# Kernel tuning notes

Hardware: AMD Instinct MI355X
Metric: run time of the kernel (lower is better)

The kernel has to match this reference:

```python
import jax, jax.numpy as jnp
import numpy as np

P = 8192          # number of gaussians
H = 256           # image height
W = 256           # image width
TANX = 0.5        # tan(fovx/2)
TANY = 0.5        # tan(fovy/2)
SCALE_MOD = 1.0
CHUNK = 128       # gaussians composited per scan step
FX = W / (2.0 * TANX)   # focal_x, as in forward()
FY = H / (2.0 * TANY)   # focal_y


def setup_inputs() -> dict:
    key = jax.random.key(0)
    k = jax.random.split(key, 6)
    # place gaussians in the camera frustum (camera at origin, looking +z)
    z = jax.random.uniform(k[0], (P,), minval=2.0, maxval=6.0)
    xy = jax.random.normal(k[1], (P, 2)) * 0.4 * (z * TANX)[:, None]
    means3D = jnp.concatenate([xy, z[:, None]], axis=1)
    scales = 0.01 + 0.04 * jax.random.uniform(k[2], (P, 3))
    rotations = jax.random.normal(k[3], (P, 4))  # normalized inside reference
    opacities = 0.05 + 0.9 * jax.random.uniform(k[4], (P, 1))
    colors_precomp = jax.random.uniform(k[5], (P, 3))
    background = jnp.zeros((3,), jnp.float32)
    viewmatrix = jnp.eye(4, dtype=jnp.float32)  # row-vector convention: p' = [p,1] @ V
    znear, zfar = 0.01, 100.0
    Pm = np.zeros((4, 4), np.float32)
    Pm[0, 0] = 1.0 / TANX
    Pm[1, 1] = 1.0 / TANY
    Pm[2, 2] = zfar / (zfar - znear)
    Pm[2, 3] = -(zfar * znear) / (zfar - znear)
    Pm[3, 2] = 1.0
    projmatrix = jnp.asarray(Pm.T)  # row-vector convention (full proj = proj @ view, view = I)
    return dict(means3D=means3D, colors_precomp=colors_precomp, opacities=opacities,
                scales=scales, rotations=rotations, background=background,
                viewmatrix=viewmatrix, projmatrix=projmatrix)


def _quat_to_rot(q):
    q = q / jnp.linalg.norm(q, axis=-1, keepdims=True)
    r, x, y, z = q[:, 0], q[:, 1], q[:, 2], q[:, 3]
    R = jnp.stack([
        1 - 2 * (y * y + z * z), 2 * (x * y - r * z), 2 * (x * z + r * y),
        2 * (x * y + r * z), 1 - 2 * (x * x + z * z), 2 * (y * z - r * x),
        2 * (x * z - r * y), 2 * (y * z + r * x), 1 - 2 * (x * x + y * y)], axis=-1)
    return R.reshape(-1, 3, 3)


def _forward(means3D, colors_precomp, opacities, scales, rotations, background,
             viewmatrix, projmatrix):
    Pn = means3D.shape[0]
    # --- preprocess: 3D covariance from scale/rotation ---
    R = _quat_to_rot(rotations)
    s2 = (scales * SCALE_MOD) ** 2
    Sigma = jnp.einsum('pij,pj,pkj->pik', R, s2, R)  # R diag(s^2) R^T, [P,3,3]
    hom = jnp.concatenate([means3D, jnp.ones((Pn, 1), means3D.dtype)], axis=1)
    p_view = (hom @ viewmatrix)[:, :3]
    p_hom = hom @ projmatrix
    p_proj = p_hom[:, :3] / (p_hom[:, 3:4] + 1e-7)
    # NDC -> pixel centers
    mean2d = jnp.stack([((p_proj[:, 0] + 1.0) * W - 1.0) * 0.5,
                        ((p_proj[:, 1] + 1.0) * H - 1.0) * 0.5], axis=1)
    depths = p_view[:, 2]
    # --- EWA splatting: project covariance to 2D ---
    Rv = viewmatrix[:3, :3]
    cov_cam = jnp.einsum('ji,pjk,kl->pil', Rv, Sigma, Rv)  # Rv^T Sigma Rv
    tz = p_view[:, 2]
    tx = jnp.clip(p_view[:, 0] / tz, -1.3 * TANX, 1.3 * TANX) * tz
    ty = jnp.clip(p_view[:, 1] / tz, -1.3 * TANY, 1.3 * TANY) * tz
    zero = jnp.zeros_like(tz)
    J = jnp.stack([jnp.stack([FX / tz, zero, -FX * tx / tz ** 2], -1),
                   jnp.stack([zero, FY / tz, -FY * ty / tz ** 2], -1)], axis=1)  # [P,2,3]
    cov2d = jnp.einsum('pij,pjk,plk->pil', J, cov_cam, J)
    a = cov2d[:, 0, 0] + 0.3  # low-pass dilation as in 3DGS
    b = cov2d[:, 0, 1]
    c = cov2d[:, 1, 1] + 0.3
    det = a * c - b * b
    conic = jnp.stack([c, -b, a], axis=-1) / det[:, None]
    # --- global depth sort ---
    order = jnp.argsort(depths)
    m2d = mean2d[order]
    con = conic[order]
    col = colors_precomp[order]
    op = opacities[order]
    # --- per-pixel front-to-back alpha compositing ---
    px, py = jnp.meshgrid(jnp.arange(W, dtype=jnp.float32),
                          jnp.arange(H, dtype=jnp.float32))
    pixf = jnp.stack([px.ravel(), py.ravel()], axis=-1)  # [HW,2]
    n_chunks = Pn // CHUNK
    xs = (m2d.reshape(n_chunks, CHUNK, 2), con.reshape(n_chunks, CHUNK, 3),
          col.reshape(n_chunks, CHUNK, 3), op.reshape(n_chunks, CHUNK, 1))

    def step(carry, x):
        accum, T = carry
        m, cn, cl, o = x
        d = m[:, None, :] - pixf[None]  # [C,HW,2]
        power = (-0.5 * (cn[:, 0:1] * d[..., 0] ** 2 + cn[:, 2:3] * d[..., 1] ** 2)
                 - cn[:, 1:2] * d[..., 0] * d[..., 1])
        alpha = jnp.minimum(0.99, o * jnp.exp(power))
        alpha = jnp.where((power > 0.0) | (alpha < 1.0 / 255.0), 0.0, alpha)
        cp = jnp.cumprod(1.0 - alpha, axis=0)  # within-chunk transmittance
        excl = jnp.concatenate([jnp.ones((1, alpha.shape[1]), alpha.dtype), cp[:-1]], 0)
        wgt = alpha * excl * T[None]
        accum = accum + jnp.einsum('cp,cd->pd', wgt, cl)
        return (accum, T * cp[-1]), None

    accum0 = jnp.zeros((H * W, 3), jnp.float32)
    T0 = jnp.ones((H * W,), jnp.float32)
    (accum, T), _ = jax.lax.scan(step, (accum0, T0), xs)
    out = accum + T[:, None] * background[None]
    return out.reshape(H, W, 3).transpose(2, 0, 1)  # [3,H,W]


def reference(means3D, colors_precomp, opacities, scales, rotations, background,
              viewmatrix, projmatrix):
    return _forward(means3D, colors_precomp, opacities, scales, rotations,
                    background, viewmatrix, projmatrix)
```

## Files before the change

### kernel.cpp

```cpp
#include <hip/hip_runtime.h>


#define PN 8192
#define IH 256
#define IW 256


__global__ __launch_bounds__(256) void preprocess_kernel(
    const float* __restrict__ means, const float* __restrict__ colors,
    const float* __restrict__ ops, const float* __restrict__ scales,
    const float* __restrict__ rots, const float* __restrict__ V,
    const float* __restrict__ Pm, float* __restrict__ ws)
{
    int i = blockIdx.x * 256 + threadIdx.x;
    if (i >= PN) return;

    float mx3 = means[3 * i], my3 = means[3 * i + 1], mz3 = means[3 * i + 2];
    float qr = rots[4 * i], qx = rots[4 * i + 1], qy = rots[4 * i + 2], qz = rots[4 * i + 3];
    float qn = 1.0f / sqrtf(qr * qr + qx * qx + qy * qy + qz * qz);
    float r = qr * qn, x = qx * qn, y = qy * qn, z = qz * qn;

    float R00 = 1.f - 2.f * (y * y + z * z), R01 = 2.f * (x * y - r * z), R02 = 2.f * (x * z + r * y);
    float R10 = 2.f * (x * y + r * z), R11 = 1.f - 2.f * (x * x + z * z), R12 = 2.f * (y * z - r * x);
    float R20 = 2.f * (x * z - r * y), R21 = 2.f * (y * z + r * x), R22 = 1.f - 2.f * (x * x + y * y);

    float s0 = scales[3 * i];     s0 *= s0;
    float s1 = scales[3 * i + 1]; s1 *= s1;
    float s2 = scales[3 * i + 2]; s2 *= s2;

    float Sg[3][3];
    Sg[0][0] = R00 * R00 * s0 + R01 * R01 * s1 + R02 * R02 * s2;
    Sg[0][1] = R00 * R10 * s0 + R01 * R11 * s1 + R02 * R12 * s2;
    Sg[0][2] = R00 * R20 * s0 + R01 * R21 * s1 + R02 * R22 * s2;
    Sg[1][1] = R10 * R10 * s0 + R11 * R11 * s1 + R12 * R12 * s2;
    Sg[1][2] = R10 * R20 * s0 + R11 * R21 * s1 + R12 * R22 * s2;
    Sg[2][2] = R20 * R20 * s0 + R21 * R21 * s1 + R22 * R22 * s2;
    Sg[1][0] = Sg[0][1]; Sg[2][0] = Sg[0][2]; Sg[2][1] = Sg[1][2];

    float pv0 = mx3 * V[0] + my3 * V[4] + mz3 * V[8]  + V[12];
    float pv1 = mx3 * V[1] + my3 * V[5] + mz3 * V[9]  + V[13];
    float pv2 = mx3 * V[2] + my3 * V[6] + mz3 * V[10] + V[14];
    float ph0 = mx3 * Pm[0] + my3 * Pm[4] + mz3 * Pm[8]  + Pm[12];
    float ph1 = mx3 * Pm[1] + my3 * Pm[5] + mz3 * Pm[9]  + Pm[13];
    float ph3 = mx3 * Pm[3] + my3 * Pm[7] + mz3 * Pm[11] + Pm[15];
    float pw = 1.0f / (ph3 + 1e-7f);
    float m2x = ((ph0 * pw + 1.0f) * (float)IW - 1.0f) * 0.5f;
    float m2y = ((ph1 * pw + 1.0f) * (float)IH - 1.0f) * 0.5f;

    float Rv[3][3];
#pragma unroll
    for (int rr = 0; rr < 3; ++rr)
#pragma unroll
        for (int cc2 = 0; cc2 < 3; ++cc2) Rv[rr][cc2] = V[rr * 4 + cc2];
    float M[3][3];
#pragma unroll
    for (int j = 0; j < 3; ++j)
#pragma unroll
        for (int l = 0; l < 3; ++l)
            M[j][l] = Sg[j][0] * Rv[0][l] + Sg[j][1] * Rv[1][l] + Sg[j][2] * Rv[2][l];
    float cc[3][3];
#pragma unroll
    for (int ii = 0; ii < 3; ++ii)
#pragma unroll
        for (int l = 0; l < 3; ++l)
            cc[ii][l] = Rv[0][ii] * M[0][l] + Rv[1][ii] * M[1][l] + Rv[2][ii] * M[2][l];

    const float FX = 256.0f, FY = 256.0f;
    float tz = pv2;
    float itz = 1.0f / tz;
    float limx = 0.65f, limy = 0.65f;
    float txz = fminf(fmaxf(pv0 * itz, -limx), limx);
    float tyz = fminf(fmaxf(pv1 * itz, -limy), limy);
    float tx = txz * tz, ty = tyz * tz;
    float J00 = FX * itz, J02 = -FX * tx * itz * itz;
    float J11 = FY * itz, J12 = -FY * ty * itz * itz;

    float u00 = J00 * cc[0][0] + J02 * cc[2][0];
    float u01 = J00 * cc[0][1] + J02 * cc[2][1];
    float u02 = J00 * cc[0][2] + J02 * cc[2][2];
    float u11 = J11 * cc[1][1] + J12 * cc[2][1];
    float u12 = J11 * cc[1][2] + J12 * cc[2][2];
    float cov00 = u00 * J00 + u02 * J02;
    float cov01 = u01 * J11 + u02 * J12;
    float cov11 = u11 * J11 + u12 * J12;

    float a = cov00 + 0.3f;
    float b = cov01;
    float c = cov11 + 0.3f;
    float det = a * c - b * b;
    float idet = 1.0f / det;
    float cA = c * idet;
    float cB = -b * idet;
    float cC = a * idet;

    float ex = sqrtf(11.2f * a);
    float ey = sqrtf(11.2f * c);
    int x0 = max(0,  (int)floorf((m2x - ex) * 0.125f));
    int x1 = min(31, (int)floorf((m2x + ex) * 0.125f));
    int y0 = max(0,  (int)floorf((m2y - ey) * 0.125f));
    int y1 = min(31, (int)floorf((m2y + ey) * 0.125f));
    x0 = min(x0, 31); y0 = min(y0, 31); x1 = max(x1, 0); y1 = max(y1, 0);
    unsigned box = (unsigned)x0 | ((unsigned)x1 << 8) | ((unsigned)y0 << 16) | ((unsigned)y1 << 24);

    ws[i] = pv2;
    float4* preA = (float4*)(ws + PN);
    float4* preB = (float4*)(ws + 5 * PN);
    preA[i] = make_float4(m2x, m2y, cA, cB);
    preB[i] = make_float4(cC, ops[i], colors[3 * i], colors[3 * i + 1]);
    ws[9 * PN + i] = colors[3 * i + 2];
    ((unsigned*)(ws + 10 * PN))[i] = box;
}

__global__ __launch_bounds__(256) void sort_scatter_kernel(float* __restrict__ ws)
{
    const float* dep = ws;
    const float4* d4 = (const float4*)ws;
    int lane = threadIdx.x & 63;
    int wid = threadIdx.x >> 6;
    int gbase = blockIdx.x * 16 + wid * 4;

    float di0 = dep[gbase], di1 = dep[gbase + 1], di2 = dep[gbase + 2], di3 = dep[gbase + 3];
    int r0 = 0, r1 = 0, r2 = 0, r3 = 0;
#pragma unroll 4
    for (int k = 0; k < 32; ++k) {
        int j4 = k * 64 + lane;
        float4 d = d4[j4];
        int jb = j4 * 4;
        r0 += (d.x < di0) || (d.x == di0 && (jb    ) < gbase);
        r0 += (d.y < di0) || (d.y == di0 && (jb + 1) < gbase);
        r0 += (d.z < di0) || (d.z == di0 && (jb + 2) < gbase);
        r0 += (d.w < di0) || (d.w == di0 && (jb + 3) < gbase);
        r1 += (d.x < di1) || (d.x == di1 && (jb    ) < gbase + 1);
        r1 += (d.y < di1) || (d.y == di1 && (jb + 1) < gbase + 1);
        r1 += (d.z < di1) || (d.z == di1 && (jb + 2) < gbase + 1);
        r1 += (d.w < di1) || (d.w == di1 && (jb + 3) < gbase + 1);
        r2 += (d.x < di2) || (d.x == di2 && (jb    ) < gbase + 2);
        r2 += (d.y < di2) || (d.y == di2 && (jb + 1) < gbase + 2);
        r2 += (d.z < di2) || (d.z == di2 && (jb + 2) < gbase + 2);
        r2 += (d.w < di2) || (d.w == di2 && (jb + 3) < gbase + 2);
        r3 += (d.x < di3) || (d.x == di3 && (jb    ) < gbase + 3);
        r3 += (d.y < di3) || (d.y == di3 && (jb + 1) < gbase + 3);
        r3 += (d.z < di3) || (d.z == di3 && (jb + 2) < gbase + 3);
        r3 += (d.w < di3) || (d.w == di3 && (jb + 3) < gbase + 3);
    }
#pragma unroll
    for (int off = 1; off < 64; off <<= 1) {
        r0 += __shfl_xor(r0, off);
        r1 += __shfl_xor(r1, off);
        r2 += __shfl_xor(r2, off);
        r3 += __shfl_xor(r3, off);
    }
    if (lane < 4) {
        int rk = (lane == 0) ? r0 : (lane == 1) ? r1 : (lane == 2) ? r2 : r3;
        int i = gbase + lane;
        const float4* preA = (const float4*)(ws + PN);
        const float4* preB = (const float4*)(ws + 5 * PN);
        float4* sA = (float4*)(ws + 11 * PN);
        float4* sB = (float4*)(ws + 15 * PN);
        sA[rk] = preA[i];
        sB[rk] = preB[i];
        ws[19 * PN + rk] = ws[9 * PN + i];
        ((unsigned*)(ws + 20 * PN))[rk] = ((const unsigned*)(ws + 10 * PN))[i];
    }
}

__global__ __launch_bounds__(512, 4) void raster_kernel(
    const float* __restrict__ ws, const float* __restrict__ bg,
    float* __restrict__ out)
{
    __shared__ float4 lsA[8][256];
    __shared__ float4 lsB[8][256];
    __shared__ float  lsb[8][256];
    volatile __shared__ float waveT[8];

    int tid = threadIdx.x;
    int lane = tid & 63, w = tid >> 6;
    int g = w >> 2, wl = w & 3;
    int yt = blockIdx.x >> 4;
    int xh = blockIdx.x & 15;
    int tileX = xh + g * 16, tileY = yt;
    int px = tileX * 8 + (lane & 7), py = tileY * 8 + (lane >> 3);
    float pxf = (float)px, pyf = (float)py;

    const float4* sA = (const float4*)(ws + 11 * PN);
    const float4* sB = (const float4*)(ws + 15 * PN);
    const float* sb = ws + 19 * PN;
    const unsigned* sbox = (const unsigned*)(ws + 20 * PN);

    if (tid < 8) waveT[tid] = 1.0f;
    __syncthreads();

    float T = 1.0f, ar = 0.0f, ag = 0.0f, ab = 0.0f;

    for (int chunk = wl * 8; chunk < wl * 8 + 8; ++chunk) {
        float pre = 1.0f;
        for (int q = g * 4; q < w; ++q) pre *= waveT[q];
        if (pre < 1e-4f) break;

        int base = chunk * 256;
        unsigned long long wv[4];
#pragma unroll
        for (int k = 0; k < 4; ++k) {
            unsigned bx = sbox[base + k * 64 + lane];
            bool ov = (tileX >= (int)(bx & 255)) & (tileX <= (int)((bx >> 8) & 255)) &
                      (tileY >= (int)((bx >> 16) & 255)) & (tileY <= (int)(bx >> 24));
            wv[k] = __ballot(ov);
        }
        if (!(wv[0] | wv[1] | wv[2] | wv[3])) continue;

        int cnt = 0;
#pragma unroll
        for (int k = 0; k < 4; ++k) {
            unsigned long long wk = wv[k];
            if ((wk >> lane) & 1ull) {
                int slot = cnt + (int)__popcll(wk & ((1ull << lane) - 1ull));
                int gg = base + k * 64 + lane;
                lsA[w][slot] = sA[gg];
                lsB[w][slot] = sB[gg];
                lsb[w][slot] = sb[gg];
            }
            cnt += (int)__popcll(wk);
        }
        asm volatile("s_waitcnt lgkmcnt(0)" ::: "memory");

        int j = 0;
        for (; j + 3 < cnt; j += 4) {
            float4 A0 = lsA[w][j],     B0 = lsB[w][j];
            float4 A1 = lsA[w][j + 1], B1 = lsB[w][j + 1];
            float4 A2 = lsA[w][j + 2], B2 = lsB[w][j + 2];
            float4 A3 = lsA[w][j + 3], B3 = lsB[w][j + 3];
            float c0 = lsb[w][j], c1 = lsb[w][j + 1], c2 = lsb[w][j + 2], c3 = lsb[w][j + 3];
            float dx0 = A0.x - pxf, dy0 = A0.y - pyf;
            float dx1 = A1.x - pxf, dy1 = A1.y - pyf;
            float dx2 = A2.x - pxf, dy2 = A2.y - pyf;
            float dx3 = A3.x - pxf, dy3 = A3.y - pyf;
            float p0 = -0.5f * (A0.z * dx0 * dx0 + B0.x * dy0 * dy0) - A0.w * dx0 * dy0;
            float p1 = -0.5f * (A1.z * dx1 * dx1 + B1.x * dy1 * dy1) - A1.w * dx1 * dy1;
            float p2 = -0.5f * (A2.z * dx2 * dx2 + B2.x * dy2 * dy2) - A2.w * dx2 * dy2;
            float p3 = -0.5f * (A3.z * dx3 * dx3 + B3.x * dy3 * dy3) - A3.w * dx3 * dy3;
            float e0 = fminf(0.99f, B0.y * __expf(p0));
            float e1 = fminf(0.99f, B1.y * __expf(p1));
            float e2 = fminf(0.99f, B2.y * __expf(p2));
            float e3 = fminf(0.99f, B3.y * __expf(p3));
            float a0 = ((p0 > 0.0f) | (e0 < (1.0f / 255.0f))) ? 0.0f : e0;
            float a1 = ((p1 > 0.0f) | (e1 < (1.0f / 255.0f))) ? 0.0f : e1;
            float a2 = ((p2 > 0.0f) | (e2 < (1.0f / 255.0f))) ? 0.0f : e2;
            float a3 = ((p3 > 0.0f) | (e3 < (1.0f / 255.0f))) ? 0.0f : e3;
            float t0 = 1.0f - a0, t1 = 1.0f - a1, t2 = 1.0f - a2, t3 = 1.0f - a3;
            float c01 = t0 * t1, c012 = c01 * t2;
            float w0 = a0 * T;
            float w1 = a1 * (T * t0);
            float w2 = a2 * (T * c01);
            float w3 = a3 * (T * c012);
            ar = fmaf(w0, B0.z, ar); ar = fmaf(w1, B1.z, ar);
            ar = fmaf(w2, B2.z, ar); ar = fmaf(w3, B3.z, ar);
            ag = fmaf(w0, B0.w, ag); ag = fmaf(w1, B1.w, ag);
            ag = fmaf(w2, B2.w, ag); ag = fmaf(w3, B3.w, ag);
            ab = fmaf(w0, c0, ab);   ab = fmaf(w1, c1, ab);
            ab = fmaf(w2, c2, ab);   ab = fmaf(w3, c3, ab);
            T *= (c012 * t3);
        }
        for (; j < cnt; ++j) {
            float4 A = lsA[w][j];
            float4 B = lsB[w][j];
            float bcol = lsb[w][j];
            float dx = A.x - pxf, dy = A.y - pyf;
            float power = -0.5f * (A.z * dx * dx + B.x * dy * dy) - A.w * dx * dy;
            float alpha = fminf(0.99f, B.y * __expf(power));
            float a2 = ((power > 0.0f) | (alpha < (1.0f / 255.0f))) ? 0.0f : alpha;
            float wgt = a2 * T;
            ar = fmaf(wgt, B.z, ar);
            ag = fmaf(wgt, B.w, ag);
            ab = fmaf(wgt, bcol, ab);
            T *= (1.0f - a2);
        }
        asm volatile("s_waitcnt lgkmcnt(0)" ::: "memory");

        if (__all(T < 1e-5f)) break;

        float tmax = T;
#pragma unroll
        for (int off = 1; off < 64; off <<= 1) tmax = fmaxf(tmax, __shfl_xor(tmax, off));
        if (lane == 0) waveT[w] = tmax;
    }

    lsb[w][lane * 4 + 0] = ar;
    lsb[w][lane * 4 + 1] = ag;
    lsb[w][lane * 4 + 2] = ab;
    lsb[w][lane * 4 + 3] = T;
    __syncthreads();

    if (wl == 0) {
        float A0 = 0.f, A1 = 0.f, A2 = 0.f, Tt = 1.f;
#pragma unroll
        for (int q = 0; q < 4; ++q) {
            A0 += Tt * lsb[g * 4 + q][lane * 4 + 0];
            A1 += Tt * lsb[g * 4 + q][lane * 4 + 1];
            A2 += Tt * lsb[g * 4 + q][lane * 4 + 2];
            Tt *= lsb[g * 4 + q][lane * 4 + 3];
        }
        int pidx = py * IW + px;
        out[pidx]               = A0 + Tt * bg[0];
        out[IH * IW + pidx]     = A1 + Tt * bg[1];
        out[2 * IH * IW + pidx] = A2 + Tt * bg[2];
    }
}

extern "C" void kernel_launch(void* const* d_in, const int* in_sizes, int n_in,
                              void* d_out, int out_size, void* d_ws, size_t ws_size,
                              hipStream_t stream) {
    const float* means  = (const float*)d_in[0];
    const float* colors = (const float*)d_in[1];
    const float* ops    = (const float*)d_in[2];
    const float* scales = (const float*)d_in[3];
    const float* rots   = (const float*)d_in[4];
    const float* bg     = (const float*)d_in[5];
    const float* viewm  = (const float*)d_in[6];
    const float* projm  = (const float*)d_in[7];
    float* out = (float*)d_out;
    float* ws  = (float*)d_ws;

    hipLaunchKernelGGL(preprocess_kernel, dim3(PN / 256), dim3(256), 0, stream,
                       means, colors, ops, scales, rots, viewm, projm, ws);
    hipLaunchKernelGGL(sort_scatter_kernel, dim3(PN / 16), dim3(256), 0, stream, ws);
    hipLaunchKernelGGL(raster_kernel, dim3(512), dim3(512), 0, stream, ws, bg, out);
}
```

Measured before the change: 106.4 us.

## Precompute per-tile gaussian bitmasks with atomics instead of per-chunk bbox tests

```diff
diff --git a/kernel.cpp b/kernel.cpp
--- a/kernel.cpp
+++ b/kernel.cpp
@@ -5,6 +5,8 @@
 #define IH 256
 #define IW 256
 
+
+#define WS_MASK (21 * PN)
 
 __global__ __launch_bounds__(256) void preprocess_kernel(
     const float* __restrict__ means, const float* __restrict__ colors,
@@ -14,6 +16,13 @@
 {
     int i = blockIdx.x * 256 + threadIdx.x;
     if (i >= PN) return;
+
+    {
+        float4 z = make_float4(0.f, 0.f, 0.f, 0.f);
+        float4* mz = (float4*)(ws + WS_MASK) + i * 8;
+#pragma unroll
+        for (int k = 0; k < 8; ++k) mz[k] = z;
+    }
 
     float mx3 = means[3 * i], my3 = means[3 * i + 1], mz3 = means[3 * i + 2];
     float qr = rots[4 * i], qx = rots[4 * i + 1], qy = rots[4 * i + 2], qz = rots[4 * i + 3];
@@ -150,6 +159,7 @@
         r2 += __shfl_xor(r2, off);
         r3 += __shfl_xor(r3, off);
     }
+
     if (lane < 4) {
         int rk = (lane == 0) ? r0 : (lane == 1) ? r1 : (lane == 2) ? r2 : r3;
         int i = gbase + lane;
@@ -160,7 +170,25 @@
         sA[rk] = preA[i];
         sB[rk] = preB[i];
         ws[19 * PN + rk] = ws[9 * PN + i];
-        ((unsigned*)(ws + 20 * PN))[rk] = ((const unsigned*)(ws + 10 * PN))[i];
+    }
+
+    const unsigned* prebox = (const unsigned*)(ws + 10 * PN);
+    unsigned long long* msk = (unsigned long long*)(ws + WS_MASK);
+    int rks[4] = {r0, r1, r2, r3};
+#pragma unroll
+    for (int j = 0; j < 4; ++j) {
+        unsigned bx = prebox[gbase + j];
+        int x0 = (int)(bx & 255), x1 = (int)((bx >> 8) & 255);
+        int y0 = (int)((bx >> 16) & 255), y1 = (int)(bx >> 24);
+        int nx = x1 - x0 + 1;
+        int n = nx * (y1 - y0 + 1);
+        int rk = rks[j];
+        unsigned long long bit = 1ull << (rk & 63);
+        int word = rk >> 6;
+        for (int t = lane; t < n; t += 64) {
+            int tyi = y0 + t / nx, txi = x0 + t % nx;
+            atomicOr(&msk[(tyi * 32 + txi) * 128 + word], bit);
+        }
     }
 }
 
@@ -179,35 +207,39 @@
     int yt = blockIdx.x >> 4;
     int xh = blockIdx.x & 15;
     int tileX = xh + g * 16, tileY = yt;
+    int tileIdx = tileY * 32 + tileX;
     int px = tileX * 8 + (lane & 7), py = tileY * 8 + (lane >> 3);
     float pxf = (float)px, pyf = (float)py;
 
     const float4* sA = (const float4*)(ws + 11 * PN);
     const float4* sB = (const float4*)(ws + 15 * PN);
     const float* sb = ws + 19 * PN;
-    const unsigned* sbox = (const unsigned*)(ws + 20 * PN);
+    const unsigned long long* wm =
+        (const unsigned long long*)(ws + WS_MASK) + (size_t)tileIdx * 128 + wl * 32;
 
     if (tid < 8) waveT[tid] = 1.0f;
     __syncthreads();
 
     float T = 1.0f, ar = 0.0f, ag = 0.0f, ab = 0.0f;
 
-    for (int chunk = wl * 8; chunk < wl * 8 + 8; ++chunk) {
+    unsigned long long m0 = wm[0], m1 = wm[1], m2 = wm[2], m3 = wm[3];
+
+    for (int c = 0; c < 8; ++c) {
+        unsigned long long wv[4] = {m0, m1, m2, m3};
+        if (c + 1 < 8) {
+            m0 = wm[(c + 1) * 4 + 0];
+            m1 = wm[(c + 1) * 4 + 1];
+            m2 = wm[(c + 1) * 4 + 2];
+            m3 = wm[(c + 1) * 4 + 3];
+        }
+
         float pre = 1.0f;
         for (int q = g * 4; q < w; ++q) pre *= waveT[q];
         if (pre < 1e-4f) break;
 
-        int base = chunk * 256;
-        unsigned long long wv[4];
-#pragma unroll
-        for (int k = 0; k < 4; ++k) {
-            unsigned bx = sbox[base + k * 64 + lane];
-            bool ov = (tileX >= (int)(bx & 255)) & (tileX <= (int)((bx >> 8) & 255)) &
-                      (tileY >= (int)((bx >> 16) & 255)) & (tileY <= (int)(bx >> 24));
-            wv[k] = __ballot(ov);
-        }
         if (!(wv[0] | wv[1] | wv[2] | wv[3])) continue;
 
+        int base = (wl * 8 + c) * 256;
         int cnt = 0;
 #pragma unroll
         for (int k = 0; k < 4; ++k) {
```

Result: slower. 109.9 us (+3.3%).
